# Kernel tuning notes

Hardware: AMD Instinct MI355X
Metric: run time of the kernel (lower is better)

Reference implementation:

```python
import jax, jax.numpy as jnp
import numpy as np

D_MODEL = 1024
HEADS = 16
D_HEAD = D_MODEL // HEADS
B, S = 2, 2048
NEG_INF = -1e9
LN_EPS = 1e-6


def setup_inputs() -> dict:
    key = jax.random.key(0)
    ks = jax.random.split(key, 10)
    q = jax.random.normal(ks[0], (B, S, D_MODEL), dtype=jnp.float32)
    k = jax.random.normal(ks[1], (B, S, D_MODEL), dtype=jnp.float32)
    v = jax.random.normal(ks[2], (B, S, D_MODEL), dtype=jnp.float32)
    sen_len = jnp.clip(jax.random.randint(ks[3], (B,), 1, S + 1), 1, S).astype(jnp.int32)
    # xavier_uniform for square matrices: limit = sqrt(6/(fan_in+fan_out))
    lim = float(np.sqrt(6.0 / (D_MODEL + D_MODEL)))
    Wq = jax.random.uniform(ks[4], (D_MODEL, D_MODEL), jnp.float32, -lim, lim)
    Wk = jax.random.uniform(ks[5], (D_MODEL, D_MODEL), jnp.float32, -lim, lim)
    Wv = jax.random.uniform(ks[6], (D_MODEL, D_MODEL), jnp.float32, -lim, lim)
    Wo = jax.random.uniform(ks[7], (D_MODEL, D_MODEL), jnp.float32, -lim, lim)
    gamma = jnp.ones((D_MODEL,), jnp.float32)
    beta = jnp.zeros((D_MODEL,), jnp.float32)
    return {"q": q, "k": k, "v": v, "Wq": Wq, "Wk": Wk, "Wv": Wv,
            "Wo": Wo, "gamma": gamma, "beta": beta, "sen_len": sen_len}


def _split_heads(x):
    # (B,S,D) -> (B,H,S,d)
    b, s, _ = x.shape
    return x.reshape(b, s, HEADS, D_HEAD).transpose(0, 2, 1, 3)


def reference(q, k, v, Wq, Wk, Wv, Wo, gamma, beta, sen_len):
    residual = q
    # torch Linear (no bias): y = x @ W.T
    qh = _split_heads(q @ Wq.T)   # (B,H,S,d)
    kh = _split_heads(k @ Wk.T)
    vh = _split_heads(v @ Wv.T)

    scores = jnp.einsum("bhqd,bhkd->bhqk", qh, kh) / jnp.sqrt(jnp.float32(D_HEAD))
    pos = jnp.arange(S)
    causal = pos[:, None] >= pos[None, :]                       # (S,S) j<=i
    pad = pos[None, :] < sen_len[:, None]                       # (B,S) key within sentence
    valid = causal[None, None, :, :] & pad[:, None, None, :]    # (B,1,S,S)
    scores = jnp.where(valid, scores, NEG_INF)

    att = jax.nn.softmax(scores, axis=-1)
    ctx = jnp.einsum("bhqk,bhkd->bhqd", att, vh)                # (B,H,S,d)
    ctx = ctx.transpose(0, 2, 1, 3).reshape(q.shape[0], S, D_MODEL)

    out = ctx @ Wo.T
    # dropout is identity at inference
    out = out + residual
    mean = jnp.mean(out, axis=-1, keepdims=True)
    var = jnp.mean(jnp.square(out - mean), axis=-1, keepdims=True)
    out = (out - mean) / jnp.sqrt(var + LN_EPS) * gamma + beta
    return out
```

## Files before the change

### kernel.cpp

```cpp
#include <hip/hip_runtime.h>

#define SEQ 2048
#define DM  1024
#define NH  16
#define DH  64

typedef __attribute__((ext_vector_type(8))) __bf16 bf16x8;
typedef __attribute__((ext_vector_type(4))) float f32x4;

__device__ inline unsigned short f2b(float f) {
  union { float f; unsigned u; } a; a.f = f;
  unsigned u = a.u;
  u += 0x7fffu + ((u >> 16) & 1u);
  return (unsigned short)(u >> 16);
}

__device__ inline void glds16(const void* g, void* s) {
  __builtin_amdgcn_global_load_lds((const __attribute__((address_space(1))) void*)g,
                                   (__attribute__((address_space(3))) void*)s,
                                   16, 0, 0);
}

__global__ __launch_bounds__(256) void cvt_all(
    const float* __restrict__ q, const float* __restrict__ k,
    const float* __restrict__ v, const float* __restrict__ Wq,
    const float* __restrict__ Wk, const float* __restrict__ Wv,
    const float* __restrict__ Wo, unsigned short* __restrict__ qb,
    unsigned short* __restrict__ kb, unsigned short* __restrict__ vb,
    unsigned short* __restrict__ Wqb, unsigned short* __restrict__ Wkb,
    unsigned short* __restrict__ Wvb, unsigned short* __restrict__ Wob) {
  int blk = blockIdx.x;
  const float* src;
  unsigned short* dst;
  int rel;
  if (blk < 4096)        { src = q;  dst = qb;  rel = blk; }
  else if (blk < 8192)   { src = k;  dst = kb;  rel = blk - 4096; }
  else if (blk < 12288)  { src = v;  dst = vb;  rel = blk - 8192; }
  else if (blk < 13312)  { src = Wq; dst = Wqb; rel = blk - 12288; }
  else if (blk < 14336)  { src = Wk; dst = Wkb; rel = blk - 13312; }
  else if (blk < 15360)  { src = Wv; dst = Wvb; rel = blk - 14336; }
  else                   { src = Wo; dst = Wob; rel = blk - 15360; }
  int i = rel * 256 + threadIdx.x;
  float4 val = ((const float4*)src)[i];
  ushort4 o;
  o.x = f2b(val.x); o.y = f2b(val.y); o.z = f2b(val.z); o.w = f2b(val.w);
  ((ushort4*)dst)[i] = o;
}

template<int MODE>
__device__ inline void gemm_body(const unsigned short* __restrict__ A,
                                 const unsigned short* __restrict__ Bt,
                                 void* __restrict__ Cv, int N, int K,
                                 unsigned short* As, unsigned short* Bs) {
  const int tid = threadIdx.x;
  const int wave = tid >> 6, lane = tid & 63;
  const int quad = lane >> 4, l16 = lane & 15;
  const int m0 = blockIdx.y * 128, n0 = blockIdx.x * 128;
  const int wm = (wave >> 1) * 64, wn = (wave & 1) * 64;
  const int srow = lane >> 3, scol = (lane & 7) * 8;

  f32x4 acc[4][4];
#pragma unroll
  for (int i = 0; i < 4; i++)
#pragma unroll
    for (int j = 0; j < 4; j++) acc[i][j] = (f32x4)0.f;

  for (int k0 = 0; k0 < K; k0 += 64) {
#pragma unroll
    for (int c = 0; c < 4; c++) {
      int inst = wave * 4 + c;
      int row = inst * 8 + srow;
      glds16(A + (size_t)(m0 + row) * K + k0 + scol, &As[inst * 512]);
      glds16(Bt + (size_t)(n0 + row) * K + k0 + scol, &Bs[inst * 512]);
    }
    __syncthreads();
#pragma unroll
    for (int ks = 0; ks < 2; ks++) {
      bf16x8 af[4], bfr[4];
#pragma unroll
      for (int i = 0; i < 4; i++)
        af[i] = *(const bf16x8*)&As[(wm + i * 16 + l16) * 64 + ks * 32 + quad * 8];
#pragma unroll
      for (int j = 0; j < 4; j++)
        bfr[j] = *(const bf16x8*)&Bs[(wn + j * 16 + l16) * 64 + ks * 32 + quad * 8];
#pragma unroll
      for (int i = 0; i < 4; i++)
#pragma unroll
        for (int j = 0; j < 4; j++)
          acc[i][j] = __builtin_amdgcn_mfma_f32_16x16x32_bf16(af[i], bfr[j],
                                                              acc[i][j], 0, 0, 0);
    }
    __syncthreads();
  }
#pragma unroll
  for (int i = 0; i < 4; i++)
#pragma unroll
    for (int j = 0; j < 4; j++)
#pragma unroll
      for (int r = 0; r < 4; r++) {
        int row = m0 + wm + i * 16 + quad * 4 + r;
        int col = n0 + wn + j * 16 + l16;
        if (MODE == 0) {
          ((unsigned short*)Cv)[(size_t)row * N + col] = f2b(acc[i][j][r]);
        } else if (MODE == 1) {
          ((float*)Cv)[(size_t)row * N + col] = acc[i][j][r];
        } else if (MODE == 2) {
          int b = row >> 11, s = row & 2047;
          int h = col >> 6, d = col & 63;
          size_t off = (((size_t)(b * NH + h) * 32 + (s >> 6)) * 8 +
                        ((s >> 4) & 3) * 2 + (d >> 5)) * 512 +
                       (((d >> 3) & 3) * 16 + (s & 15)) * 8 + (d & 7);
          ((unsigned short*)Cv)[off] = f2b(acc[i][j][r]);
        } else {
          int b = row >> 11, s = row & 2047, jj = s & 63;
          int h = col >> 6, d = col & 63;
          size_t off = (((size_t)(b * NH + h) * 32 + (s >> 6)) * 8 +
                        (jj >> 5) * 4 + (d >> 4)) * 512 +
                       (((jj >> 3) & 3) * 16 + (d & 15)) * 8 + (jj & 7);
          ((unsigned short*)Cv)[off] = f2b(acc[i][j][r]);
        }
      }
}

__global__ __launch_bounds__(256) void gemm_qkv(
    const unsigned short* __restrict__ A0, const unsigned short* __restrict__ A1,
    const unsigned short* __restrict__ A2, const unsigned short* __restrict__ B0,
    const unsigned short* __restrict__ B1, const unsigned short* __restrict__ B2,
    unsigned short* __restrict__ C0, unsigned short* __restrict__ C1,
    unsigned short* __restrict__ C2) {
  __shared__ unsigned short As[128 * 64];
  __shared__ unsigned short Bs[128 * 64];
  if (blockIdx.z == 0)      gemm_body<0>(A0, B0, (void*)C0, DM, DM, As, Bs);
  else if (blockIdx.z == 1) gemm_body<2>(A1, B1, (void*)C1, DM, DM, As, Bs);
  else                      gemm_body<3>(A2, B2, (void*)C2, DM, DM, As, Bs);
}

__global__ __launch_bounds__(256) void gemm_out(const unsigned short* __restrict__ A,
                                                const unsigned short* __restrict__ Bt,
                                                float* __restrict__ C) {
  __shared__ unsigned short As[128 * 64];
  __shared__ unsigned short Bs[128 * 64];
  gemm_body<1>(A, Bt, (void*)C, DM, DM, As, Bs);
}

__global__ __launch_bounds__(64) void attn_kernel(const unsigned short* __restrict__ Qp,
                                                  const unsigned short* __restrict__ Ksw,
                                                  const unsigned short* __restrict__ Vsw,
                                                  const int* __restrict__ sen_len,
                                                  unsigned short* __restrict__ ctx) {
  __shared__ unsigned int Pl[16 * 36];

  const int lane = threadIdx.x;
  const int quad = lane >> 4, l16 = lane & 15;
  const int bh = blockIdx.x, b = bh >> 4, h = bh & 15;
  const int qt = 127 - (int)blockIdx.y;
  const int slen = sen_len[b];
  const int qrow = qt * 16 + l16;

  const size_t qbase = ((size_t)b * SEQ + qrow) * DM + h * DH;
  bf16x8 qf0 = *(const bf16x8*)(Qp + qbase + quad * 8);
  bf16x8 qf1 = *(const bf16x8*)(Qp + qbase + 32 + quad * 8);

  const unsigned short* kbase = Ksw + (size_t)bh * 32 * 4096 + lane * 8;
  const unsigned short* vbase = Vsw + (size_t)bh * 32 * 4096 + lane * 8;
  const unsigned short* Pw16 = (const unsigned short*)Pl;

  int jend = qt * 16 + 16;
  if (slen < jend) jend = slen;
  const int nch = (jend + 63) >> 6;

  float m = -1e30f, l = 0.f;
  f32x4 o[4];
#pragma unroll
  for (int i = 0; i < 4; i++) o[i] = (f32x4)0.f;

  bf16x8 ka[4][2];
#pragma unroll
  for (int fi = 0; fi < 8; fi++)
    ka[fi >> 1][fi & 1] = *(const bf16x8*)(kbase + fi * 512);

  for (int c = 0; c < nch; ++c) {
    const int j0 = c * 64;
    bf16x8 vf[2][4];
#pragma unroll
    for (int fi = 0; fi < 8; fi++)
      vf[fi >> 2][fi & 3] = *(const bf16x8*)(vbase + (size_t)c * 4096 + fi * 512);
    const int cn = (c + 1 < nch) ? c + 1 : c;
    bf16x8 kn[4][2];
#pragma unroll
    for (int fi = 0; fi < 8; fi++)
      kn[fi >> 1][fi & 1] = *(const bf16x8*)(kbase + (size_t)cn * 4096 + fi * 512);

    f32x4 sacc[4];
#pragma unroll
    for (int kt = 0; kt < 4; kt++) sacc[kt] = (f32x4)0.f;
#pragma unroll
    for (int kt = 0; kt < 4; kt++) {
      sacc[kt] = __builtin_amdgcn_mfma_f32_16x16x32_bf16(ka[kt][0], qf0, sacc[kt], 0, 0, 0);
      sacc[kt] = __builtin_amdgcn_mfma_f32_16x16x32_bf16(ka[kt][1], qf1, sacc[kt], 0, 0, 0);
    }
    float cmax = -1e30f;
#pragma unroll
    for (int kt = 0; kt < 4; kt++)
#pragma unroll
      for (int r = 0; r < 4; r++) {
        int j = j0 + kt * 16 + quad * 4 + r;
        float v = (j <= qrow && j < slen) ? sacc[kt][r] * 0.125f : -1e30f;
        sacc[kt][r] = v;
        cmax = fmaxf(cmax, v);
      }
    cmax = fmaxf(cmax, __shfl_xor(cmax, 16));
    cmax = fmaxf(cmax, __shfl_xor(cmax, 32));
    float mnew = fmaxf(m, cmax);
    float alpha = __expf(m - mnew);
    float psum = 0.f;
#pragma unroll
    for (int kt = 0; kt < 4; kt++)
#pragma unroll
      for (int rp = 0; rp < 2; rp++) {
        float p0 = __expf(sacc[kt][2 * rp] - mnew);
        float p1 = __expf(sacc[kt][2 * rp + 1] - mnew);
        psum += p0 + p1;
        Pl[l16 * 36 + kt * 8 + quad * 2 + rp] =
            (unsigned)f2b(p0) | ((unsigned)f2b(p1) << 16);
      }
    psum += __shfl_xor(psum, 16);
    psum += __shfl_xor(psum, 32);
    l = l * alpha + psum;
    m = mnew;
#pragma unroll
    for (int r = 0; r < 4; r++) {
      float ar = __shfl(alpha, quad * 4 + r);
#pragma unroll
      for (int ni = 0; ni < 4; ni++) o[ni][r] *= ar;
    }
#pragma unroll
    for (int ko = 0; ko < 2; ko++) {
      bf16x8 pf = *(const bf16x8*)&Pw16[l16 * 72 + ko * 32 + quad * 8];
#pragma unroll
      for (int ni = 0; ni < 4; ni++)
        o[ni] = __builtin_amdgcn_mfma_f32_16x16x32_bf16(pf, vf[ko][ni], o[ni], 0, 0, 0);
    }
#pragma unroll
    for (int fi = 0; fi < 8; fi++) ka[fi >> 1][fi & 1] = kn[fi >> 1][fi & 1];
  }

#pragma unroll
  for (int r = 0; r < 4; r++) {
    float lr = __shfl(l, quad * 4 + r);
    float inv = 1.0f / lr;
    int row = qt * 16 + quad * 4 + r;
#pragma unroll
    for (int ni = 0; ni < 4; ni++) {
      float v = o[ni][r] * inv;
      ctx[((size_t)b * SEQ + row) * DM + h * DH + ni * 16 + l16] = f2b(v);
    }
  }
}

__global__ __launch_bounds__(256) void ln_kernel(const float* __restrict__ xp,
                                                 const float* __restrict__ resid,
                                                 const float* __restrict__ gamma,
                                                 const float* __restrict__ beta,
                                                 float* __restrict__ out) {
  const int row = blockIdx.x;
  const int tid = threadIdx.x;
  const size_t base = (size_t)row * DM + tid * 4;
  float4 x = *(const float4*)(xp + base);
  float4 rv = *(const float4*)(resid + base);
  x.x += rv.x; x.y += rv.y; x.z += rv.z; x.w += rv.w;
  float s = x.x + x.y + x.z + x.w;
  float s2 = x.x * x.x + x.y * x.y + x.z * x.z + x.w * x.w;
#pragma unroll
  for (int off = 1; off < 64; off <<= 1) {
    s += __shfl_xor(s, off);
    s2 += __shfl_xor(s2, off);
  }
  __shared__ float sm[4], sm2[4];
  const int wave = tid >> 6, lane = tid & 63;
  if (lane == 0) { sm[wave] = s; sm2[wave] = s2; }
  __syncthreads();
  s = sm[0] + sm[1] + sm[2] + sm[3];
  s2 = sm2[0] + sm2[1] + sm2[2] + sm2[3];
  float mean = s * (1.f / 1024.f);
  float var = s2 * (1.f / 1024.f) - mean * mean;
  float rstd = rsqrtf(var + 1e-6f);
  float4 g = *(const float4*)(gamma + tid * 4);
  float4 bt = *(const float4*)(beta + tid * 4);
  float4 o;
  o.x = (x.x - mean) * rstd * g.x + bt.x;
  o.y = (x.y - mean) * rstd * g.y + bt.y;
  o.z = (x.z - mean) * rstd * g.z + bt.z;
  o.w = (x.w - mean) * rstd * g.w + bt.w;
  *(float4*)(out + base) = o;
}

extern "C" void kernel_launch(void* const* d_in, const int* in_sizes, int n_in,
                              void* d_out, int out_size, void* d_ws, size_t ws_size,
                              hipStream_t stream) {
  const float* q     = (const float*)d_in[0];
  const float* k     = (const float*)d_in[1];
  const float* v     = (const float*)d_in[2];
  const float* Wq    = (const float*)d_in[3];
  const float* Wk    = (const float*)d_in[4];
  const float* Wv    = (const float*)d_in[5];
  const float* Wo    = (const float*)d_in[6];
  const float* gamma = (const float*)d_in[7];
  const float* beta  = (const float*)d_in[8];
  const int* sen_len = (const int*)d_in[9];
  float* out = (float*)d_out;

  char* ws = (char*)d_ws;
  const size_t MB = (size_t)1 << 20;
  if (ws_size < 64 * MB) return;
  unsigned short* qb  = (unsigned short*)(ws + 0 * MB);
  unsigned short* kb  = (unsigned short*)(ws + 8 * MB);
  unsigned short* vb  = (unsigned short*)(ws + 16 * MB);
  unsigned short* Wqb = (unsigned short*)(ws + 24 * MB);
  unsigned short* Wkb = (unsigned short*)(ws + 26 * MB);
  unsigned short* Wvb = (unsigned short*)(ws + 28 * MB);
  unsigned short* Wob = (unsigned short*)(ws + 30 * MB);
  unsigned short* Qp  = (unsigned short*)(ws + 32 * MB);
  unsigned short* Ksw = (unsigned short*)(ws + 40 * MB);
  unsigned short* Vsw = (unsigned short*)(ws + 48 * MB);
  unsigned short* ctx = (unsigned short*)(ws + 56 * MB);
  float* outp = (float*)(ws + 8 * MB);

  cvt_all<<<16384, 256, 0, stream>>>(q, k, v, Wq, Wk, Wv, Wo,
                                     qb, kb, vb, Wqb, Wkb, Wvb, Wob);

  gemm_qkv<<<dim3(8, 32, 3), 256, 0, stream>>>(qb, kb, vb, Wqb, Wkb, Wvb,
                                               Qp, Ksw, Vsw);

  attn_kernel<<<dim3(32, 128), 64, 0, stream>>>(Qp, Ksw, Vsw, sen_len, ctx);

  gemm_out<<<dim3(8, 32), 256, 0, stream>>>(ctx, Wob, outp);

  ln_kernel<<<4096, 256, 0, stream>>>(outp, q, gamma, beta, out);
}
```

Before: 245.5 us.

## Process two query tiles per attention wave and reorder GEMM block mapping

The attention kernel now has each 64-lane block handle two adjacent 16-row query tiles, so every K and V chunk loaded from memory feeds both tiles and global K/V traffic per query row is halved. The earlier register prefetch of the next K chunk is dropped in favour of loading K and V inside the loop, and the grid shrinks to half as many blocks. The GEMM kernels swap grid dimensions so consecutive block IDs walk along M rather than N, which changes L2 reuse of the weight tiles. The cost is higher register pressure and fewer waves for the attention kernel, and the lost K prefetch may expose load latency.

```diff
diff --git a/kernel.cpp b/kernel.cpp
--- a/kernel.cpp
+++ b/kernel.cpp
@@ -51,11 +51,12 @@
 __device__ inline void gemm_body(const unsigned short* __restrict__ A,
                                  const unsigned short* __restrict__ Bt,
                                  void* __restrict__ Cv, int N, int K,
-                                 unsigned short* As, unsigned short* Bs) {
+                                 unsigned short* As, unsigned short* Bs,
+                                 int mt, int nt) {
   const int tid = threadIdx.x;
   const int wave = tid >> 6, lane = tid & 63;
   const int quad = lane >> 4, l16 = lane & 15;
-  const int m0 = blockIdx.y * 128, n0 = blockIdx.x * 128;
+  const int m0 = mt * 128, n0 = nt * 128;
   const int wm = (wave >> 1) * 64, wn = (wave & 1) * 64;
   const int srow = lane >> 3, scol = (lane & 7) * 8;
 
@@ -130,9 +131,10 @@
     unsigned short* __restrict__ C2) {
   __shared__ unsigned short As[128 * 64];
   __shared__ unsigned short Bs[128 * 64];
-  if (blockIdx.z == 0)      gemm_body<0>(A0, B0, (void*)C0, DM, DM, As, Bs);
-  else if (blockIdx.z == 1) gemm_body<2>(A1, B1, (void*)C1, DM, DM, As, Bs);
-  else                      gemm_body<3>(A2, B2, (void*)C2, DM, DM, As, Bs);
+  const int mt = blockIdx.x, nt = blockIdx.y;
+  if (blockIdx.z == 0)      gemm_body<0>(A0, B0, (void*)C0, DM, DM, As, Bs, mt, nt);
+  else if (blockIdx.z == 1) gemm_body<2>(A1, B1, (void*)C1, DM, DM, As, Bs, mt, nt);
+  else                      gemm_body<3>(A2, B2, (void*)C2, DM, DM, As, Bs, mt, nt);
 }
 
 __global__ __launch_bounds__(256) void gemm_out(const unsigned short* __restrict__ A,
@@ -140,7 +142,7 @@
                                                 float* __restrict__ C) {
   __shared__ unsigned short As[128 * 64];
   __shared__ unsigned short Bs[128 * 64];
-  gemm_body<1>(A, Bt, (void*)C, DM, DM, As, Bs);
+  gemm_body<1>(A, Bt, (void*)C, DM, DM, As, Bs, blockIdx.x, blockIdx.y);
 }
 
 __global__ __launch_bounds__(64) void attn_kernel(const unsigned short* __restrict__ Qp,
@@ -148,114 +150,124 @@
                                                   const unsigned short* __restrict__ Vsw,
                                                   const int* __restrict__ sen_len,
                                                   unsigned short* __restrict__ ctx) {
-  __shared__ unsigned int Pl[16 * 36];
+  __shared__ unsigned int Pl[2][16 * 36];
 
   const int lane = threadIdx.x;
   const int quad = lane >> 4, l16 = lane & 15;
   const int bh = blockIdx.x, b = bh >> 4, h = bh & 15;
-  const int qt = 127 - (int)blockIdx.y;
+  const int pair = 63 - (int)blockIdx.y;
+  const int qt0 = pair * 2;
   const int slen = sen_len[b];
-  const int qrow = qt * 16 + l16;
-
-  const size_t qbase = ((size_t)b * SEQ + qrow) * DM + h * DH;
-  bf16x8 qf0 = *(const bf16x8*)(Qp + qbase + quad * 8);
-  bf16x8 qf1 = *(const bf16x8*)(Qp + qbase + 32 + quad * 8);
+
+  int qrow[2];
+  qrow[0] = qt0 * 16 + l16;
+  qrow[1] = qt0 * 16 + 16 + l16;
+
+  bf16x8 qf[2][2];
+#pragma unroll
+  for (int sub = 0; sub < 2; sub++) {
+    const size_t qbase = ((size_t)b * SEQ + qrow[sub]) * DM + h * DH;
+    qf[sub][0] = *(const bf16x8*)(Qp + qbase + quad * 8);
+    qf[sub][1] = *(const bf16x8*)(Qp + qbase + 32 + quad * 8);
+  }
 
   const unsigned short* kbase = Ksw + (size_t)bh * 32 * 4096 + lane * 8;
   const unsigned short* vbase = Vsw + (size_t)bh * 32 * 4096 + lane * 8;
-  const unsigned short* Pw16 = (const unsigned short*)Pl;
-
-  int jend = qt * 16 + 16;
+
+  int jend = qt0 * 16 + 32;
   if (slen < jend) jend = slen;
   const int nch = (jend + 63) >> 6;
 
-  float m = -1e30f, l = 0.f;
-  f32x4 o[4];
-#pragma unroll
-  for (int i = 0; i < 4; i++) o[i] = (f32x4)0.f;
-
-  bf16x8 ka[4][2];
-#pragma unroll
-  for (int fi = 0; fi < 8; fi++)
-    ka[fi >> 1][fi & 1] = *(const bf16x8*)(kbase + fi * 512);
+  float m[2] = {-1e30f, -1e30f};
+  float lsum[2] = {0.f, 0.f};
+  f32x4 o[2][4];
+#pragma unroll
+  for (int sub = 0; sub < 2; sub++)
+#pragma unroll
+    for (int i = 0; i < 4; i++) o[sub][i] = (f32x4)0.f;
 
   for (int c = 0; c < nch; ++c) {
     const int j0 = c * 64;
-    bf16x8 vf[2][4];
+    bf16x8 ka[4][2], vf[2][4];
+#pragma unroll
+    for (int fi = 0; fi < 8; fi++)
+      ka[fi >> 1][fi & 1] = *(const bf16x8*)(kbase + (size_t)c * 4096 + fi * 512);
 #pragma unroll
     for (int fi = 0; fi < 8; fi++)
       vf[fi >> 2][fi & 3] = *(const bf16x8*)(vbase + (size_t)c * 4096 + fi * 512);
-    const int cn = (c + 1 < nch) ? c + 1 : c;
-    bf16x8 kn[4][2];
-#pragma unroll
-    for (int fi = 0; fi < 8; fi++)
-      kn[fi >> 1][fi & 1] = *(const bf16x8*)(kbase + (size_t)cn * 4096 + fi * 512);
-
-    f32x4 sacc[4];
-#pragma unroll
-    for (int kt = 0; kt < 4; kt++) sacc[kt] = (f32x4)0.f;
-#pragma unroll
-    for (int kt = 0; kt < 4; kt++) {
-      sacc[kt] = __builtin_amdgcn_mfma_f32_16x16x32_bf16(ka[kt][0], qf0, sacc[kt], 0, 0, 0);
-      sacc[kt] = __builtin_amdgcn_mfma_f32_16x16x32_bf16(ka[kt][1], qf1, sacc[kt], 0, 0, 0);
-    }
-    float cmax = -1e30f;
-#pragma unroll
-    for (int kt = 0; kt < 4; kt++)
+
+#pragma unroll
+    for (int sub = 0; sub < 2; sub++) {
+      f32x4 sacc[4];
+#pragma unroll
+      for (int kt = 0; kt < 4; kt++) sacc[kt] = (f32x4)0.f;
+#pragma unroll
+      for (int kt = 0; kt < 4; kt++) {
+        sacc[kt] = __builtin_amdgcn_mfma_f32_16x16x32_bf16(ka[kt][0], qf[sub][0],
+                                                           sacc[kt], 0, 0, 0);
+        sacc[kt] = __builtin_amdgcn_mfma_f32_16x16x32_bf16(ka[kt][1], qf[sub][1],
+                                                           sacc[kt], 0, 0, 0);
+      }
+      float cmax = -1e30f;
+#pragma unroll
+      for (int kt = 0; kt < 4; kt++)
+#pragma unroll
+        for (int r = 0; r < 4; r++) {
+          int j = j0 + kt * 16 + quad * 4 + r;
+          float v = (j <= qrow[sub] && j < slen) ? sacc[kt][r] * 0.125f : -1e30f;
+          sacc[kt][r] = v;
+          cmax = fmaxf(cmax, v);
+        }
+      cmax = fmaxf(cmax, __shfl_xor(cmax, 16));
+      cmax = fmaxf(cmax, __shfl_xor(cmax, 32));
+      float mnew = fmaxf(m[sub], cmax);
+      float alpha = __expf(m[sub] - mnew);
+      float psum = 0.f;
+#pragma unroll
+      for (int kt = 0; kt < 4; kt++)
+#pragma unroll
+        for (int rp = 0; rp < 2; rp++) {
+          float p0 = __expf(sacc[kt][2 * rp] - mnew);
+          float p1 = __expf(sacc[kt][2 * rp + 1] - mnew);
+          psum += p0 + p1;
+          Pl[sub][l16 * 36 + kt * 8 + quad * 2 + rp] =
+              (unsigned)f2b(p0) | ((unsigned)f2b(p1) << 16);
+        }
+      psum += __shfl_xor(psum, 16);
+      psum += __shfl_xor(psum, 32);
+      lsum[sub] = lsum[sub] * alpha + psum;
+      m[sub] = mnew;
 #pragma unroll
       for (int r = 0; r < 4; r++) {
-        int j = j0 + kt * 16 + quad * 4 + r;
-        float v = (j <= qrow && j < slen) ? sacc[kt][r] * 0.125f : -1e30f;
-        sacc[kt][r] = v;
-        cmax = fmaxf(cmax, v);
-      }
-    cmax = fmaxf(cmax, __shfl_xor(cmax, 16));
-    cmax = fmaxf(cmax, __shfl_xor(cmax, 32));
-    float mnew = fmaxf(m, cmax);
-    float alpha = __expf(m - mnew);
-    float psum = 0.f;
-#pragma unroll
-    for (int kt = 0; kt < 4; kt++)
-#pragma unroll
-      for (int rp = 0; rp < 2; rp++) {
-        float p0 = __expf(sacc[kt][2 * rp] - mnew);
-        float p1 = __expf(sacc[kt][2 * rp + 1] - mnew);
-        psum += p0 + p1;
-        Pl[l16 * 36 + kt * 8 + quad * 2 + rp] =
-            (unsigned)f2b(p0) | ((unsigned)f2b(p1) << 16);
-      }
-    psum += __shfl_xor(psum, 16);
-    psum += __shfl_xor(psum, 32);
-    l = l * alpha + psum;
-    m = mnew;
-#pragma unroll
-    for (int r = 0; r < 4; r++) {
-      float ar = __shfl(alpha, quad * 4 + r);
-#pragma unroll
-      for (int ni = 0; ni < 4; ni++) o[ni][r] *= ar;
-    }
-#pragma unroll
-    for (int ko = 0; ko < 2; ko++) {
-      bf16x8 pf = *(const bf16x8*)&Pw16[l16 * 72 + ko * 32 + quad * 8];
-#pragma unroll
-      for (int ni = 0; ni < 4; ni++)
-        o[ni] = __builtin_amdgcn_mfma_f32_16x16x32_bf16(pf, vf[ko][ni], o[ni], 0, 0, 0);
-    }
-#pragma unroll
-    for (int fi = 0; fi < 8; fi++) ka[fi >> 1][fi & 1] = kn[fi >> 1][fi & 1];
-  }
-
-#pragma unroll
-  for (int r = 0; r < 4; r++) {
-    float lr = __shfl(l, quad * 4 + r);
-    float inv = 1.0f / lr;
-    int row = qt * 16 + quad * 4 + r;
-#pragma unroll
-    for (int ni = 0; ni < 4; ni++) {
-      float v = o[ni][r] * inv;
-      ctx[((size_t)b * SEQ + row) * DM + h * DH + ni * 16 + l16] = f2b(v);
+        float ar = __shfl(alpha, quad * 4 + r);
+#pragma unroll
+        for (int ni = 0; ni < 4; ni++) o[sub][ni][r] *= ar;
+      }
+      const unsigned short* Pw16 = (const unsigned short*)&Pl[sub][0];
+#pragma unroll
+      for (int ko = 0; ko < 2; ko++) {
+        bf16x8 pf = *(const bf16x8*)&Pw16[l16 * 72 + ko * 32 + quad * 8];
+#pragma unroll
+        for (int ni = 0; ni < 4; ni++)
+          o[sub][ni] = __builtin_amdgcn_mfma_f32_16x16x32_bf16(pf, vf[ko][ni],
+                                                               o[sub][ni], 0, 0, 0);
+      }
     }
   }
+
+#pragma unroll
+  for (int sub = 0; sub < 2; sub++)
+#pragma unroll
+    for (int r = 0; r < 4; r++) {
+      float lr = __shfl(lsum[sub], quad * 4 + r);
+      float inv = 1.0f / lr;
+      int row = qt0 * 16 + sub * 16 + quad * 4 + r;
+#pragma unroll
+      for (int ni = 0; ni < 4; ni++) {
+        float v = o[sub][ni][r] * inv;
+        ctx[((size_t)b * SEQ + row) * DM + h * DH + ni * 16 + l16] = f2b(v);
+      }
+    }
 }
 
 __global__ __launch_bounds__(256) void ln_kernel(const float* __restrict__ xp,
@@ -329,12 +341,12 @@
   cvt_all<<<16384, 256, 0, stream>>>(q, k, v, Wq, Wk, Wv, Wo,
                                      qb, kb, vb, Wqb, Wkb, Wvb, Wob);
 
-  gemm_qkv<<<dim3(8, 32, 3), 256, 0, stream>>>(qb, kb, vb, Wqb, Wkb, Wvb,
+  gemm_qkv<<<dim3(32, 8, 3), 256, 0, stream>>>(qb, kb, vb, Wqb, Wkb, Wvb,
                                                Qp, Ksw, Vsw);
 
-  attn_kernel<<<dim3(32, 128), 64, 0, stream>>>(Qp, Ksw, Vsw, sen_len, ctx);
-
-  gemm_out<<<dim3(8, 32), 256, 0, stream>>>(ctx, Wob, outp);
+  attn_kernel<<<dim3(32, 64), 64, 0, stream>>>(Qp, Ksw, Vsw, sen_len, ctx);
+
+  gemm_out<<<dim3(32, 8), 256, 0, stream>>>(ctx, Wob, outp);
 
   ln_kernel<<<4096, 256, 0, stream>>>(outp, q, gamma, beta, out);
 }
```

Result: slower. 252.2 us (+2.7%).
